# Kernel tuning notes

Measured on AMD Instinct MI355X. Metric: run time of the kernel, lower is better.

Reference implementation:

```python
import jax, jax.numpy as jnp
import numpy as np

B, S, H = 1, 2048, 2048
NH, NKV, HD = 16, 4, 128
N_REP = NH // NKV
WINDOW = 1024
THETA = 10000.0


def _rope(x, fc):
    # x: [B,S,h,HD]; fc: [B,S,HD//2,2] (cos,sin)
    xr = x.reshape(*x.shape[:-1], HD // 2, 2)
    a, b = xr[..., 0], xr[..., 1]
    cos = fc[:, :, None, :, 0]
    sin = fc[:, :, None, :, 1]
    out = jnp.stack((a * cos - b * sin, a * sin + b * cos), axis=-1)
    return out.reshape(x.shape)


def setup_inputs() -> dict:
    key = jax.random.key(0)
    ks = jax.random.split(key, 5)
    hidden_state = jax.random.normal(ks[0], (B, S, H), jnp.float32)
    # rotary table: cos/sin of pos * theta^{-2i/d}
    inv_freq = 1.0 / (THETA ** (jnp.arange(0, HD, 2, dtype=jnp.float32) / HD))
    ang = jnp.arange(S, dtype=jnp.float32)[:, None] * inv_freq[None, :]  # [S, HD//2]
    freq_cis = jnp.stack((jnp.cos(ang), jnp.sin(ang)), axis=-1)  # [S, HD//2, 2]
    attention_mask = jnp.ones((B, S), dtype=bool)
    i = jnp.arange(S)[:, None]
    j = jnp.arange(S)[None, :]
    causal_mask = ((j <= i) & (i - j < WINDOW))[None, None]  # [1,1,S,S] sliding-window causal
    position_ids = jnp.broadcast_to(jnp.arange(S, dtype=jnp.int32), (B, S))
    scale = 0.02
    Wq = jax.random.normal(ks[1], (H, NH * HD), jnp.float32) * scale
    Wk = jax.random.normal(ks[2], (H, NKV * HD), jnp.float32) * scale
    Wv = jax.random.normal(ks[3], (H, NKV * HD), jnp.float32) * scale
    Wo = jax.random.normal(ks[4], (NH * HD, H), jnp.float32) * scale
    return {"hidden_state": hidden_state, "freq_cis": freq_cis,
            "attention_mask": attention_mask, "causal_mask": causal_mask,
            "position_ids": position_ids, "Wq": Wq, "Wk": Wk, "Wv": Wv, "Wo": Wo}


def reference(hidden_state, freq_cis, attention_mask, causal_mask, position_ids,
              Wq, Wk, Wv, Wo):
    q = (hidden_state @ Wq).reshape(B, S, NH, HD)
    k = (hidden_state @ Wk).reshape(B, S, NKV, HD)
    v = (hidden_state @ Wv).reshape(B, S, NKV, HD)
    fc = freq_cis[position_ids]  # [B,S,HD//2,2]
    q = _rope(q, fc)
    k = _rope(k, fc)
    # GQA: repeat kv heads (contiguous groups, as in repeat_kv)
    k = jnp.repeat(k, N_REP, axis=2)  # [B,S,NH,HD]
    v = jnp.repeat(v, N_REP, axis=2)
    mask = causal_mask & attention_mask[:, None, None, :]  # [B,1,S,S]
    bias = jnp.where(mask, 0.0, jnp.finfo(jnp.float32).min)
    scores = jnp.einsum('bqhd,bkhd->bhqk', q, k) * (1.0 / np.sqrt(HD))
    attn = jax.nn.softmax(scores + bias, axis=-1)
    out = jnp.einsum('bhqk,bkhd->bqhd', attn, v).reshape(B, S, NH * HD)
    return out @ Wo
```

## Files before the change

### kernel.cpp

```cpp
#include <hip/hip_runtime.h>
#include <hip/hip_bf16.h>
#include <stdint.h>

#define S_LEN 2048
#define HDIM  2048
#define NHQ   16
#define NKVH  4
#define HD    128
#define WIN   1024
#define QKV_N 3072
#define SM_SCALE 0.08838834764831845f
#define NEG_BIG  -1.0e30f

typedef __attribute__((ext_vector_type(8))) short short8;
typedef __attribute__((ext_vector_type(4))) float float4v;
typedef unsigned short u16;

static __device__ __forceinline__ float bf2f(u16 u) {
  union { unsigned int i; float f; } v; v.i = ((unsigned int)u) << 16; return v.f;
}
static __device__ __forceinline__ u16 f2bf(float f) {
  union { float f; unsigned int i; } v; v.f = f;
  unsigned int x = v.i;
  return (u16)((x + 0x7fffu + ((x >> 16) & 1u)) >> 16);
}

__global__ __launch_bounds__(256) void cvt_f32_bf16(
    const float* __restrict__ x, u16* __restrict__ y, int n)
{
  const int i = (blockIdx.x * 256 + threadIdx.x) * 4;
  if (i < n) {
    const float4 v = *(const float4*)(x + i);
    y[i + 0] = f2bf(v.x);
    y[i + 1] = f2bf(v.y);
    y[i + 2] = f2bf(v.z);
    y[i + 3] = f2bf(v.w);
  }
}

__global__ __launch_bounds__(256) void wtrans_all(
    const float* __restrict__ Wq, const float* __restrict__ Wk,
    const float* __restrict__ Wv, const float* __restrict__ Wo,
    u16* __restrict__ WqkvT, u16* __restrict__ WoT)
{
  __shared__ u16 t[32][33];
  const int tx = threadIdx.x & 31, ty = threadIdx.x >> 5;
  const int k0 = blockIdx.y * 32;

  const float* W; u16* DT; int nsrc, N;
  const int n0 = blockIdx.x * 32;
  if (blockIdx.z == 0) {
    if (n0 < 2048)      { W = Wq; nsrc = n0;        N = 2048; }
    else if (n0 < 2560) { W = Wk; nsrc = n0 - 2048; N = 512;  }
    else                { W = Wv; nsrc = n0 - 2560; N = 512;  }
    DT = WqkvT;
  } else {
    if (n0 >= 2048) return;
    W = Wo; nsrc = n0; N = 2048; DT = WoT;
  }

#pragma unroll
  for (int i = 0; i < 4; ++i)
    t[ty + i * 8][tx] = f2bf(W[(size_t)(k0 + ty + i * 8) * N + nsrc + tx]);
  __syncthreads();
#pragma unroll
  for (int i = 0; i < 4; ++i)
    DT[(size_t)(n0 + ty + i * 8) * 2048 + k0 + tx] = t[tx][ty + i * 8];
}

template <bool OUT_F32>
__global__ __launch_bounds__(256) void gemm_bt(
    const u16* __restrict__ A, const u16* __restrict__ BT,
    void* __restrict__ Cv, int M, int N, int K)
{
  __shared__ u16 Als[128 * 32];
  __shared__ u16 Bls[64 * 32];

  const int tid  = threadIdx.x;
  const int lane = tid & 63;
  const int w    = tid >> 6;
  const int quad = lane >> 4;
  const int lc   = lane & 15;
  const int n0   = blockIdx.x * 64;
  const int m0   = blockIdx.y * 128;
  const int wr   = (w >> 1) * 64;
  const int wc   = (w & 1) * 32;

  float4v acc[4][2];
#pragma unroll
  for (int i = 0; i < 4; ++i)
#pragma unroll
    for (int j = 0; j < 2; ++j) acc[i][j] = (float4v){0.f, 0.f, 0.f, 0.f};

  for (int k0 = 0; k0 < K; k0 += 32) {
    __syncthreads();
#pragma unroll
    for (int r = 0; r < 2; ++r) {
      const int off  = r * 4096 + tid * 16;
      const int row  = off >> 6;
      const int colb = off & 63;
      const u16* ga = A + (size_t)(m0 + row) * K + k0 + (colb >> 1);
      __builtin_amdgcn_global_load_lds(
          (__attribute__((address_space(1))) void*)ga,
          (__attribute__((address_space(3))) void*)((char*)Als + off), 16, 0, 0);
    }
    {
      const int off  = tid * 16;
      const int row  = off >> 6;
      const int colb = off & 63;
      const u16* gb = BT + (size_t)(n0 + row) * K + k0 + (colb >> 1);
      __builtin_amdgcn_global_load_lds(
          (__attribute__((address_space(1))) void*)gb,
          (__attribute__((address_space(3))) void*)((char*)Bls + off), 16, 0, 0);
    }
    __syncthreads();

    short8 af[4], bfr[2];
#pragma unroll
    for (int mi = 0; mi < 4; ++mi)
      af[mi] = *(const short8*)(Als + (wr + mi * 16 + lc) * 32 + quad * 8);
#pragma unroll
    for (int ni = 0; ni < 2; ++ni)
      bfr[ni] = *(const short8*)(Bls + (wc + ni * 16 + lc) * 32 + quad * 8);
#pragma unroll
    for (int mi = 0; mi < 4; ++mi)
#pragma unroll
      for (int ni = 0; ni < 2; ++ni)
        acc[mi][ni] = __builtin_amdgcn_mfma_f32_16x16x32_bf16(
            af[mi], bfr[ni], acc[mi][ni], 0, 0, 0);
  }

#pragma unroll
  for (int mi = 0; mi < 4; ++mi)
#pragma unroll
    for (int ni = 0; ni < 2; ++ni)
#pragma unroll
      for (int r = 0; r < 4; ++r) {
        const int row = m0 + wr + mi * 16 + quad * 4 + r;
        const int col = n0 + wc + ni * 16 + lc;
        if (OUT_F32)
          ((float*)Cv)[(size_t)row * N + col] = acc[mi][ni][r];
        else
          ((u16*)Cv)[(size_t)row * N + col] = f2bf(acc[mi][ni][r]);
      }
}

__global__ __launch_bounds__(256) void rope_pack(
    u16* __restrict__ qkv, const float* __restrict__ fc,
    u16* __restrict__ kp)
{
  const int b = blockIdx.x;
  if (b < 1024) {
    const int t    = b * 256 + threadIdx.x;
    const int row  = t >> 7;
    const int head = (t & 127) >> 3;
    const int d0   = (t & 7) * 8;
    u16* p = qkv + (size_t)row * QKV_N + head * HD + 2 * d0;
    short8 v0 = *(const short8*)p;
    short8 v1 = *(const short8*)(p + 8);
    const float2* f = (const float2*)(fc + row * 128) + d0;
    short8 o0, o1;
#pragma unroll
    for (int u = 0; u < 4; ++u) {
      const float2 cs = f[u];
      const float a = bf2f((u16)v0[2 * u]), bb = bf2f((u16)v0[2 * u + 1]);
      o0[2 * u]     = (short)f2bf(a * cs.x - bb * cs.y);
      o0[2 * u + 1] = (short)f2bf(a * cs.y + bb * cs.x);
    }
#pragma unroll
    for (int u = 0; u < 4; ++u) {
      const float2 cs = f[4 + u];
      const float a = bf2f((u16)v1[2 * u]), bb = bf2f((u16)v1[2 * u + 1]);
      o1[2 * u]     = (short)f2bf(a * cs.x - bb * cs.y);
      o1[2 * u + 1] = (short)f2bf(a * cs.y + bb * cs.x);
    }
    *(short8*)p = o0;
    *(short8*)(p + 8) = o1;
  } else {
    const int bb2 = b - 1024;
    const int kvh = bb2 >> 5;
    const int kt  = bb2 & 31;
    u16* dst = kp + ((size_t)(kvh * 32 + kt)) * 64 * 128;
#pragma unroll
    for (int i = 0; i < 4; ++i) {
      const int cid = i * 256 + threadIdx.x;
      const int key = cid >> 4;
      const int c   = cid & 15;
      const int s   = kt * 64 + key;
      short8 v = *(const short8*)(qkv + (size_t)s * QKV_N + 2048 + kvh * HD + c * 8);
      const float2* f = (const float2*)(fc + s * 128) + c * 4;
      short8 o;
#pragma unroll
      for (int u = 0; u < 4; ++u) {
        const float2 cs = f[u];
        const float a = bf2f((u16)v[2 * u]), bb3 = bf2f((u16)v[2 * u + 1]);
        o[2 * u]     = (short)f2bf(a * cs.x - bb3 * cs.y);
        o[2 * u + 1] = (short)f2bf(a * cs.y + bb3 * cs.x);
      }
      *(short8*)(dst + key * 128 + ((c ^ (key & 15)) * 8)) = o;
    }
  }
}

__global__ __launch_bounds__(256) void vpack_kernel(
    const u16* __restrict__ qkv, u16* __restrict__ vp)
{
  __shared__ u16 t[32][33];
  const int s0  = blockIdx.x * 32;
  const int h0  = blockIdx.y * 32;
  const int kvh = blockIdx.z;
  const int tx = threadIdx.x & 31, ty = threadIdx.x >> 5;
  const int kt   = s0 >> 6;
  const int keyb = s0 & 63;
#pragma unroll
  for (int i = 0; i < 4; ++i)
    t[ty + i * 8][tx] = qkv[(size_t)(s0 + ty + i * 8) * QKV_N + 2560 + kvh * HD + h0 + tx];
  __syncthreads();
  u16* dst = vp + ((size_t)(kvh * 32 + kt)) * 128 * 64;
#pragma unroll
  for (int i = 0; i < 4; ++i) {
    const int hd   = h0 + ty + i * 8;
    const int keyl = keyb + tx;
    const int c    = (keyl >> 3) ^ (hd & 7);
    dst[hd * 64 + c * 8 + (keyl & 7)] = t[tx][ty + i * 8];
  }
}

__global__ __launch_bounds__(256) void attn_kernel(
    const u16* __restrict__ qkv, const u16* __restrict__ kp,
    const u16* __restrict__ vp, u16* __restrict__ out)
{
  __shared__ u16 Kls[64 * 128];
  __shared__ u16 Vls[128 * 64];
  __shared__ u16 P[4 * 16 * 72];

  const int tid  = threadIdx.x;
  const int lane = tid & 63;
  const int w    = tid >> 6;
  const int quad = lane >> 4;
  const int lc   = lane & 15;
  const int q0   = blockIdx.x * 64;
  const int h    = blockIdx.y;
  const int kvh  = h >> 2;
  const int rb   = q0 + w * 16;

  short8 qf[4];
  {
    const u16* qp = qkv + (size_t)(rb + lc) * QKV_N + h * HD + quad * 8;
#pragma unroll
    for (int ks = 0; ks < 4; ++ks) qf[ks] = *(const short8*)(qp + ks * 32);
  }

  float4v o[8];
#pragma unroll
  for (int i = 0; i < 8; ++i) o[i] = (float4v){0.f, 0.f, 0.f, 0.f};
  float mrow[4], lrow[4];
#pragma unroll
  for (int r = 0; r < 4; ++r) { mrow[r] = NEG_BIG; lrow[r] = 0.f; }

  int jmin_blk = q0 - (WIN - 1); if (jmin_blk < 0) jmin_blk = 0;
  const int kt_begin = jmin_blk >> 6;
  const int kt_end   = q0 >> 6;

  const size_t tbase = (size_t)(kvh * 32) * 64 * 128;

  for (int kt = kt_begin; kt <= kt_end; ++kt) {
    const int k0 = kt * 64;

    __syncthreads();
    {
      const u16* kg = kp + tbase + (size_t)kt * 64 * 128;
      const u16* vg = vp + tbase + (size_t)kt * 128 * 64;
#pragma unroll
      for (int i = 0; i < 4; ++i) {
        const int off = i * 4096 + tid * 16;
        __builtin_amdgcn_global_load_lds(
            (__attribute__((address_space(1))) void*)((const char*)kg + off),
            (__attribute__((address_space(3))) void*)((char*)Kls + off), 16, 0, 0);
        __builtin_amdgcn_global_load_lds(
            (__attribute__((address_space(1))) void*)((const char*)vg + off),
            (__attribute__((address_space(3))) void*)((char*)Vls + off), 16, 0, 0);
      }
    }
    __syncthreads();

    if (k0 > rb + 15 || k0 + 63 < rb - (WIN - 1)) continue;

    float4v sacc[4];
#pragma unroll
    for (int i = 0; i < 4; ++i) sacc[i] = (float4v){0.f, 0.f, 0.f, 0.f};
#pragma unroll
    for (int ks = 0; ks < 4; ++ks) {
#pragma unroll
      for (int nt = 0; nt < 4; ++nt) {
        const int key = nt * 16 + lc;
        const int c   = (ks * 4 + quad) ^ (key & 15);
        short8 kb = *(const short8*)(Kls + key * 128 + c * 8);
        sacc[nt] = __builtin_amdgcn_mfma_f32_16x16x32_bf16(qf[ks], kb, sacc[nt], 0, 0, 0);
      }
    }

    const bool full = (k0 + 63 <= rb) && ((rb + 15 - k0) <= WIN - 1);
    float sv[4][4];
    bool  ok[4][4];
    float rmax[4] = {NEG_BIG, NEG_BIG, NEG_BIG, NEG_BIG};
#pragma unroll
    for (int nt = 0; nt < 4; ++nt) {
      const int j = k0 + nt * 16 + lc;
#pragma unroll
      for (int r = 0; r < 4; ++r) {
        const int i = rb + quad * 4 + r;
        const bool valid = full || ((j <= i) && (i - j < WIN));
        float s = sacc[nt][r] * SM_SCALE;
        s = valid ? s : NEG_BIG;
        sv[nt][r] = s;
        ok[nt][r] = valid;
        rmax[r] = fmaxf(rmax[r], s);
      }
    }
#pragma unroll
    for (int off = 1; off < 16; off <<= 1)
#pragma unroll
      for (int r = 0; r < 4; ++r)
        rmax[r] = fmaxf(rmax[r], __shfl_xor(rmax[r], off, 64));

    float alpha[4], rsum[4];
#pragma unroll
    for (int r = 0; r < 4; ++r) {
      const float mn = fmaxf(mrow[r], rmax[r]);
      alpha[r] = __expf(mrow[r] - mn);
      mrow[r] = mn;
      rsum[r] = 0.f;
    }
#pragma unroll
    for (int nt = 0; nt < 4; ++nt)
#pragma unroll
      for (int r = 0; r < 4; ++r) {
        const float p = ok[nt][r] ? __expf(sv[nt][r] - mrow[r]) : 0.f;
        rsum[r] += p;
        P[(w * 16 + quad * 4 + r) * 72 + nt * 16 + lc] = f2bf(p);
      }
#pragma unroll
    for (int off = 1; off < 16; off <<= 1)
#pragma unroll
      for (int r = 0; r < 4; ++r)
        rsum[r] += __shfl_xor(rsum[r], off, 64);
#pragma unroll
    for (int r = 0; r < 4; ++r) lrow[r] = lrow[r] * alpha[r] + rsum[r];
#pragma unroll
    for (int i = 0; i < 8; ++i)
#pragma unroll
      for (int r = 0; r < 4; ++r) o[i][r] *= alpha[r];

#pragma unroll
    for (int ktk = 0; ktk < 2; ++ktk) {
      short8 pa = *(const short8*)(P + (w * 16 + lc) * 72 + ktk * 32 + quad * 8);
#pragma unroll
      for (int nt2 = 0; nt2 < 8; ++nt2) {
        const int hd = nt2 * 16 + lc;
        const int c  = (ktk * 4 + quad) ^ (hd & 7);
        short8 vb = *(const short8*)(Vls + hd * 64 + c * 8);
        o[nt2] = __builtin_amdgcn_mfma_f32_16x16x32_bf16(pa, vb, o[nt2], 0, 0, 0);
      }
    }
  }

#pragma unroll
  for (int r = 0; r < 4; ++r) {
    const float inv = (lrow[r] > 0.f) ? (1.f / lrow[r]) : 0.f;
#pragma unroll
    for (int nt2 = 0; nt2 < 8; ++nt2) {
      const int row = rb + quad * 4 + r;
      const int col = h * HD + nt2 * 16 + lc;
      out[(size_t)row * 2048 + col] = f2bf(o[nt2][r] * inv);
    }
  }
}

extern "C" void kernel_launch(void* const* d_in, const int* in_sizes, int n_in,
                              void* d_out, int out_size, void* d_ws, size_t ws_size,
                              hipStream_t stream) {
  const float* hs = (const float*)d_in[0];
  const float* fc = (const float*)d_in[1];
  const float* Wq = (const float*)d_in[5];
  const float* Wk = (const float*)d_in[6];
  const float* Wv = (const float*)d_in[7];
  const float* Wo = (const float*)d_in[8];
  float* outp = (float*)d_out;

  u16* hsB   = (u16*)d_ws;
  u16* WqkvT = hsB   + (size_t)2048 * 2048;
  u16* WoT   = WqkvT + (size_t)3072 * 2048;
  u16* QKV   = WoT   + (size_t)2048 * 2048;
  u16* ATTN  = QKV   + (size_t)2048 * 3072;
  u16* Kp    = ATTN  + (size_t)2048 * 2048;
  u16* Vp    = Kp    + (size_t)4 * 2048 * 128;

  dim3 blk(256);
  cvt_f32_bf16<<<dim3(2048 * 2048 / 1024), blk, 0, stream>>>(hs, hsB, 2048 * 2048);
  wtrans_all<<<dim3(96, 64, 2), blk, 0, stream>>>(Wq, Wk, Wv, Wo, WqkvT, WoT);

  gemm_bt<false><<<dim3(3072 / 64, 2048 / 128), blk, 0, stream>>>(hsB, WqkvT, QKV, 2048, 3072, 2048);
  rope_pack<<<dim3(1152), blk, 0, stream>>>(QKV, fc, Kp);
  vpack_kernel<<<dim3(64, 4, NKVH), blk, 0, stream>>>(QKV, Vp);
  attn_kernel<<<dim3(2048 / 64, NHQ), blk, 0, stream>>>(QKV, Kp, Vp, ATTN);
  gemm_bt<true><<<dim3(2048 / 64, 2048 / 128), blk, 0, stream>>>(ATTN, WoT, outp, 2048, 2048, 2048);
}
```

Before: 273.2 us.

## Pre-pack GEMM operands into tile-contiguous k-chunk-major layout for LDS loads

Adds a tile-packed layout for the GEMM A and B operands: each 128x32 (A) or 64x32 (B) k-tile is stored contiguously with k-chunk-major ordering. The hidden-state conversion, the weight transpose and the attention output writer now emit this layout directly. Each GEMM tile load becomes a single contiguous stream, and LDS fragment reads become row-strided-by-8 so they avoid bank conflicts. The cost is more scattered writes in the producer kernels, especially the attention epilogue's 2-byte stores.

```diff
diff --git a/kernel.cpp b/kernel.cpp
--- a/kernel.cpp
+++ b/kernel.cpp
@@ -25,16 +25,26 @@
   return (u16)((x + 0x7fffu + ((x >> 16) & 1u)) >> 16);
 }
 
-__global__ __launch_bounds__(256) void cvt_f32_bf16(
-    const float* __restrict__ x, u16* __restrict__ y, int n)
-{
-  const int i = (blockIdx.x * 256 + threadIdx.x) * 4;
-  if (i < n) {
-    const float4 v = *(const float4*)(x + i);
-    y[i + 0] = f2bf(v.x);
-    y[i + 1] = f2bf(v.y);
-    y[i + 2] = f2bf(v.z);
-    y[i + 3] = f2bf(v.w);
+__global__ __launch_bounds__(256) void hs_pack(
+    const float* __restrict__ x, u16* __restrict__ y)
+{
+  const int b = blockIdx.x;
+  u16* dst = y + (size_t)b * 4096;
+  const int mb = b >> 6, ks = b & 63;
+#pragma unroll
+  for (int i = 0; i < 2; ++i) {
+    const int cid = i * 256 + threadIdx.x;
+    const int kc  = cid & 3;
+    const int m   = cid >> 2;
+    const float* src = x + ((size_t)(mb * 128 + m)) * 2048 + ks * 32 + kc * 8;
+    const float4 v0 = *(const float4*)src;
+    const float4 v1 = *(const float4*)(src + 4);
+    short8 o;
+    o[0] = (short)f2bf(v0.x); o[1] = (short)f2bf(v0.y);
+    o[2] = (short)f2bf(v0.z); o[3] = (short)f2bf(v0.w);
+    o[4] = (short)f2bf(v1.x); o[5] = (short)f2bf(v1.y);
+    o[6] = (short)f2bf(v1.z); o[7] = (short)f2bf(v1.w);
+    *(short8*)(dst + (kc * 128 + m) * 8) = o;
   }
 }
 
@@ -46,9 +56,9 @@
   __shared__ u16 t[32][33];
   const int tx = threadIdx.x & 31, ty = threadIdx.x >> 5;
   const int k0 = blockIdx.y * 32;
+  const int n0 = blockIdx.x * 32;
 
   const float* W; u16* DT; int nsrc, N;
-  const int n0 = blockIdx.x * 32;
   if (blockIdx.z == 0) {
     if (n0 < 2048)      { W = Wq; nsrc = n0;        N = 2048; }
     else if (n0 < 2560) { W = Wk; nsrc = n0 - 2048; N = 512;  }
@@ -63,18 +73,23 @@
   for (int i = 0; i < 4; ++i)
     t[ty + i * 8][tx] = f2bf(W[(size_t)(k0 + ty + i * 8) * N + nsrc + tx]);
   __syncthreads();
-#pragma unroll
-  for (int i = 0; i < 4; ++i)
-    DT[(size_t)(n0 + ty + i * 8) * 2048 + k0 + tx] = t[tx][ty + i * 8];
+  const int kstep = blockIdx.y;
+  const int kc = tx >> 3, e = tx & 7;
+#pragma unroll
+  for (int i = 0; i < 4; ++i) {
+    const int n = n0 + ty + i * 8;
+    DT[((size_t)((n >> 6) * 64 + kstep)) * 2048 + kc * 512 + (n & 63) * 8 + e]
+        = t[tx][ty + i * 8];
+  }
 }
 
 template <bool OUT_F32>
 __global__ __launch_bounds__(256) void gemm_bt(
-    const u16* __restrict__ A, const u16* __restrict__ BT,
+    const u16* __restrict__ Apk, const u16* __restrict__ Bpk,
     void* __restrict__ Cv, int M, int N, int K)
 {
-  __shared__ u16 Als[128 * 32];
-  __shared__ u16 Bls[64 * 32];
+  __shared__ u16 Als[4096];
+  __shared__ u16 Bls[2048];
 
   const int tid  = threadIdx.x;
   const int lane = tid & 63;
@@ -85,6 +100,7 @@
   const int m0   = blockIdx.y * 128;
   const int wr   = (w >> 1) * 64;
   const int wc   = (w & 1) * 32;
+  const int ktiles = K >> 5;
 
   float4v acc[4][2];
 #pragma unroll
@@ -92,25 +108,21 @@
 #pragma unroll
     for (int j = 0; j < 2; ++j) acc[i][j] = (float4v){0.f, 0.f, 0.f, 0.f};
 
-  for (int k0 = 0; k0 < K; k0 += 32) {
+  for (int ks = 0; ks < ktiles; ++ks) {
+    const char* ab = (const char*)(Apk + ((size_t)((m0 >> 7) * ktiles + ks)) * 4096);
+    const char* bb = (const char*)(Bpk + ((size_t)((n0 >> 6) * ktiles + ks)) * 2048);
     __syncthreads();
 #pragma unroll
     for (int r = 0; r < 2; ++r) {
-      const int off  = r * 4096 + tid * 16;
-      const int row  = off >> 6;
-      const int colb = off & 63;
-      const u16* ga = A + (size_t)(m0 + row) * K + k0 + (colb >> 1);
+      const int off = r * 4096 + tid * 16;
       __builtin_amdgcn_global_load_lds(
-          (__attribute__((address_space(1))) void*)ga,
+          (__attribute__((address_space(1))) void*)(ab + off),
           (__attribute__((address_space(3))) void*)((char*)Als + off), 16, 0, 0);
     }
     {
-      const int off  = tid * 16;
-      const int row  = off >> 6;
-      const int colb = off & 63;
-      const u16* gb = BT + (size_t)(n0 + row) * K + k0 + (colb >> 1);
+      const int off = tid * 16;
       __builtin_amdgcn_global_load_lds(
-          (__attribute__((address_space(1))) void*)gb,
+          (__attribute__((address_space(1))) void*)(bb + off),
           (__attribute__((address_space(3))) void*)((char*)Bls + off), 16, 0, 0);
     }
     __syncthreads();
@@ -118,10 +130,10 @@
     short8 af[4], bfr[2];
 #pragma unroll
     for (int mi = 0; mi < 4; ++mi)
-      af[mi] = *(const short8*)(Als + (wr + mi * 16 + lc) * 32 + quad * 8);
+      af[mi] = *(const short8*)(Als + quad * 1024 + (wr + mi * 16 + lc) * 8);
 #pragma unroll
     for (int ni = 0; ni < 2; ++ni)
-      bfr[ni] = *(const short8*)(Bls + (wc + ni * 16 + lc) * 32 + quad * 8);
+      bfr[ni] = *(const short8*)(Bls + quad * 512 + (wc + ni * 16 + lc) * 8);
 #pragma unroll
     for (int mi = 0; mi < 4; ++mi)
 #pragma unroll
@@ -368,11 +380,14 @@
 #pragma unroll
   for (int r = 0; r < 4; ++r) {
     const float inv = (lrow[r] > 0.f) ? (1.f / lrow[r]) : 0.f;
+    const int row = rb + quad * 4 + r;
+    const size_t mbase = (size_t)(row >> 7) * 64;
+    const int m = row & 127;
 #pragma unroll
     for (int nt2 = 0; nt2 < 8; ++nt2) {
-      const int row = rb + quad * 4 + r;
       const int col = h * HD + nt2 * 16 + lc;
-      out[(size_t)row * 2048 + col] = f2bf(o[nt2][r] * inv);
+      const int kstep = col >> 5, kc = (col >> 3) & 3, e = col & 7;
+      out[(mbase + kstep) * 4096 + kc * 1024 + m * 8 + e] = f2bf(o[nt2][r] * inv);
     }
   }
 }
@@ -397,7 +412,7 @@
   u16* Vp    = Kp    + (size_t)4 * 2048 * 128;
 
   dim3 blk(256);
-  cvt_f32_bf16<<<dim3(2048 * 2048 / 1024), blk, 0, stream>>>(hs, hsB, 2048 * 2048);
+  hs_pack<<<dim3(1024), blk, 0, stream>>>(hs, hsB);
   wtrans_all<<<dim3(96, 64, 2), blk, 0, stream>>>(Wq, Wk, Wv, Wo, WqkvT, WoT);
 
   gemm_bt<false><<<dim3(3072 / 64, 2048 / 128), blk, 0, stream>>>(hsB, WqkvT, QKV, 2048, 3072, 2048);
```

After: 265.7 us. -2.7%, faster.
